# Kernel tuning notes

Measured on AMD Instinct MI355X. Metric: run time of the kernel, lower is better.

## Reference

```python
import jax, jax.numpy as jnp
import numpy as np
import math

B, S, D, H = 2, 2048, 1024, 16
HD = D // H
WINDOW_LEFT = 256   # window_size=(256,-1): only left constraint active
NEG = -1e9


def rotate_half(x):
    x1, x2 = jnp.split(x, 2, axis=-1)
    return jnp.concatenate([-x2, x1], axis=-1)


def setup_inputs() -> dict:
    key = jax.random.key(0)
    ks = jax.random.split(key, 10)
    x = jax.random.normal(ks[0], (B, S, D), dtype=jnp.float32)
    mask = jnp.ones((B, S), dtype=bool)
    cos = jax.random.uniform(ks[1], (B, S, HD), dtype=jnp.float32)
    sin = jax.random.uniform(ks[2], (B, S, HD), dtype=jnp.float32)
    sc = 1.0 / math.sqrt(D)
    Wq = jax.random.normal(ks[3], (D, D), dtype=jnp.float32) * sc
    bq = jax.random.normal(ks[4], (D,), dtype=jnp.float32) * 0.02
    Wk = jax.random.normal(ks[5], (D, D), dtype=jnp.float32) * sc
    Wv = jax.random.normal(ks[6], (D, D), dtype=jnp.float32) * sc
    bv = jax.random.normal(ks[7], (D,), dtype=jnp.float32) * 0.02
    Wo = jax.random.normal(ks[8], (D, D), dtype=jnp.float32) * sc
    bo = jax.random.normal(ks[9], (D,), dtype=jnp.float32) * 0.02
    return {"x": x, "mask": mask, "cos": cos, "sin": sin,
            "Wq": Wq, "bq": bq, "Wk": Wk, "Wv": Wv, "bv": bv,
            "Wo": Wo, "bo": bo}


def reference(x, mask, cos, sin, Wq, bq, Wk, Wv, bv, Wo, bo):
    batch, seq_len, embed_dim = x.shape
    scale = 1.0 / math.sqrt(HD)

    q = x @ Wq + bq          # [b,s,d], bias on q
    k = x @ Wk               # no bias on k
    v = x @ Wv + bv          # bias on v

    def split_heads(t):
        return jnp.swapaxes(t.reshape(batch, seq_len, H, HD), 1, 2)  # [b,h,s,hd]

    q, k, v = split_heads(q), split_heads(k), split_heads(v)

    c = cos[:, None, :, :]   # [b,1,s,hd]
    s_ = sin[:, None, :, :]
    q = q * c + rotate_half(q) * s_
    k = k * c + rotate_half(k) * s_

    scores = jnp.einsum('bhqd,bhkd->bhqk', q, k) * scale
    # padding mask over keys
    scores = jnp.where(mask[:, None, None, :], scores, NEG)
    # causal + sliding-window (left=256) masks combined
    pos = jnp.arange(seq_len)
    rel = pos[None, :] - pos[:, None]          # k - q
    keep = (rel <= 0) & (rel >= -WINDOW_LEFT)  # causal AND window-left
    scores = jnp.where(keep, scores, NEG)

    weights = jax.nn.softmax(scores, axis=-1)
    context = jnp.einsum('bhqk,bhkd->bhqd', weights, v)
    context = jnp.swapaxes(context, 1, 2).reshape(batch, seq_len, embed_dim)
    out = context @ Wo + bo
    out = out * mask[..., None]
    return out
```

## Files before the change

### kernel.cpp

```cpp
#include <hip/hip_runtime.h>
#include <cstdint>
#include <cstddef>

typedef __bf16 bf16;
typedef bf16 bf16x4 __attribute__((ext_vector_type(4)));
typedef bf16 bf16x8 __attribute__((ext_vector_type(8)));
typedef float f32x4 __attribute__((ext_vector_type(4)));

#define S_LEN 2048
#define DIM   1024
#define NHEAD 16
#define HDIM  64

__device__ __forceinline__ f32x4 mfma16(bf16x8 a, bf16x8 b, f32x4 c) {
    return __builtin_amdgcn_mfma_f32_16x16x32_bf16(a, b, c, 0, 0, 0);
}

__device__ __forceinline__ float exp2fast(float x) {
    return __builtin_amdgcn_exp2f(x);
}

__device__ __forceinline__ void gload_lds16(const bf16* g, bf16* l) {
    __builtin_amdgcn_global_load_lds(
        (const __attribute__((address_space(1))) unsigned*)g,
        (__attribute__((address_space(3))) unsigned*)l, 16, 0, 0);
}

__global__ __launch_bounds__(256) void cvt_x_kernel(const float* __restrict__ x,
                                                    bf16* __restrict__ xb) {
    int i = blockIdx.x * 256 + threadIdx.x;
    float4 v = ((const float4*)x)[i];
    bf16x4 o = { (bf16)v.x, (bf16)v.y, (bf16)v.z, (bf16)v.w };
    ((bf16x4*)xb)[i] = o;
}

__global__ __launch_bounds__(256) void wt_kernel(const float* __restrict__ Wq, const float* __restrict__ Wk,
                                                 const float* __restrict__ Wv, const float* __restrict__ Wo,
                                                 bf16* __restrict__ WqT, bf16* __restrict__ WkT,
                                                 bf16* __restrict__ WvT, bf16* __restrict__ WoT) {
    const float* W; bf16* WT;
    int z = blockIdx.z;
    if      (z == 0) { W = Wq; WT = WqT; }
    else if (z == 1) { W = Wk; WT = WkT; }
    else if (z == 2) { W = Wv; WT = WvT; }
    else             { W = Wo; WT = WoT; }
    __shared__ bf16 tile[64][72];
    int k0 = blockIdx.x * 64, n0 = blockIdx.y * 64;
    int t = threadIdx.x;
#pragma unroll
    for (int p = 0; p < 4; ++p) {
        int task = p * 256 + t;
        int ki = task >> 4, nj = (task & 15) * 4;
        float4 v = *(const float4*)(W + (size_t)(k0 + ki) * DIM + n0 + nj);
        tile[ki][nj + 0] = (bf16)v.x; tile[ki][nj + 1] = (bf16)v.y;
        tile[ki][nj + 2] = (bf16)v.z; tile[ki][nj + 3] = (bf16)v.w;
    }
    __syncthreads();
#pragma unroll
    for (int p = 0; p < 4; ++p) {
        int task = p * 256 + t;
        int ni = task >> 4, kj = (task & 15) * 4;
        bf16x4 o = { tile[kj + 0][ni], tile[kj + 1][ni], tile[kj + 2][ni], tile[kj + 3][ni] };
        *(bf16x4*)(WT + (size_t)(n0 + ni) * DIM + k0 + kj) = o;
    }
}

__device__ __forceinline__ void stage_tile(const bf16* __restrict__ A, const bf16* __restrict__ BT,
                                           int m0, int n0, int k0,
                                           bf16* sA, bf16* sB, int w, int lane) {
#pragma unroll
    for (int p = 0; p < 2; ++p) {
        int c = p * 256 + w * 64 + lane;
        const bf16* ga = A + (size_t)(m0 + (c >> 2)) * DIM + k0 + (c & 3) * 8;
        gload_lds16(ga, sA + (p * 256 + w * 64) * 8);
        const bf16* gb = BT + (size_t)(n0 + (c >> 2)) * DIM + k0 + (c & 3) * 8;
        gload_lds16(gb, sB + (p * 256 + w * 64) * 8);
    }
}

__device__ __forceinline__ void gemm_main(const bf16* __restrict__ A, const bf16* __restrict__ BT,
                                          int m0, int n0, f32x4 acc[4][4]) {
    __shared__ bf16 sA[3][128 * 32];
    __shared__ bf16 sB[3][128 * 32];
    int t = threadIdx.x;
    int lane = t & 63, w = t >> 6;
    int wr = w >> 1, wc = w & 1;
    int lc = lane & 15, lr = lane >> 4;
    const int NSTEP = DIM / 32;

    stage_tile(A, BT, m0, n0, 0,  sA[0], sB[0], w, lane);
    stage_tile(A, BT, m0, n0, 32, sA[1], sB[1], w, lane);

    int rs = 0, ss = 2;
    for (int kt = 0; kt < NSTEP; ++kt) {
        if (kt < NSTEP - 1) asm volatile("s_waitcnt vmcnt(4)" ::: "memory");
        else                asm volatile("s_waitcnt vmcnt(0)" ::: "memory");
        __builtin_amdgcn_s_barrier();
        asm volatile("" ::: "memory");
        if (kt < NSTEP - 2)
            stage_tile(A, BT, m0, n0, (kt + 2) * 32, sA[ss], sB[ss], w, lane);

        const bf16* pa = sA[rs] + (wr * 64 + lc) * 32 + lr * 8;
        const bf16* pb = sB[rs] + (wc * 64 + lc) * 32 + lr * 8;
        bf16x8 af[4], bfr[4];
#pragma unroll
        for (int m = 0; m < 4; ++m) af[m] = *(const bf16x8*)(pa + m * 16 * 32);
#pragma unroll
        for (int n = 0; n < 4; ++n) bfr[n] = *(const bf16x8*)(pb + n * 16 * 32);
#pragma unroll
        for (int m = 0; m < 4; ++m)
#pragma unroll
            for (int n = 0; n < 4; ++n)
                acc[m][n] = mfma16(af[m], bfr[n], acc[m][n]);
        rs = (rs == 2) ? 0 : rs + 1;
        ss = (ss == 2) ? 0 : ss + 1;
    }
}

__global__ __launch_bounds__(256, 3) void gemm_qkv_kernel(const bf16* __restrict__ xb,
                                                          const bf16* __restrict__ WqT, const bf16* __restrict__ WkT,
                                                          const bf16* __restrict__ WvT,
                                                          const float* __restrict__ bq, const float* __restrict__ bv,
                                                          const float* __restrict__ cosp, const float* __restrict__ sinp,
                                                          bf16* __restrict__ qT, bf16* __restrict__ kT,
                                                          bf16* __restrict__ vT) {
    int z = blockIdx.z;
    const bf16* BT = (z == 0) ? WqT : (z == 1) ? WkT : WvT;
    int m0 = blockIdx.x * 128, n0 = blockIdx.y * 128;
    f32x4 acc[4][4] = {};
    gemm_main(xb, BT, m0, n0, acc);

    int t = threadIdx.x;
    int lane = t & 63, w = t >> 6;
    int wr = w >> 1, wc = w & 1;
    int lc = lane & 15, lr = lane >> 4;
    int row0 = m0 + wr * 64 + lr * 4;
    int h = (n0 >> 6) + wc;

    if (z < 2) {
        bf16* qkT = (z == 0) ? qT : kT;
#pragma unroll
        for (int nf = 0; nf < 2; ++nf) {
            int hd1 = lc + nf * 16;
            int c1i = h * HDIM + hd1;
            float b1 = (z == 0) ? bq[c1i] : 0.0f;
            float b2 = (z == 0) ? bq[c1i + 32] : 0.0f;
#pragma unroll
            for (int mf = 0; mf < 4; ++mf) {
#pragma unroll
                for (int r = 0; r < 4; ++r) {
                    int bs = row0 + mf * 16 + r;
                    size_t cb = (size_t)bs * HDIM + hd1;
                    float c1 = cosp[cb], s1 = sinp[cb];
                    float c2 = cosp[cb + 32], s2 = sinp[cb + 32];
                    float v1 = acc[mf][nf][r] + b1;
                    float v2 = acc[mf][nf + 2][r] + b2;
                    int b = bs >> 11, s = bs & (S_LEN - 1);
                    size_t o = ((size_t)(b * NHEAD + h) * S_LEN + s) * HDIM;
                    qkT[o + hd1]      = (bf16)(v1 * c1 - v2 * s1);
                    qkT[o + hd1 + 32] = (bf16)(v2 * c2 + v1 * s2);
                }
            }
        }
    } else {
#pragma unroll
        for (int nf = 0; nf < 4; ++nf) {
            int hd = lc + nf * 16;
            float bvv = bv[h * HDIM + hd];
#pragma unroll
            for (int mf = 0; mf < 4; ++mf) {
                bf16x4 o;
#pragma unroll
                for (int r = 0; r < 4; ++r) o[r] = (bf16)(acc[mf][nf][r] + bvv);
                int bs = row0 + mf * 16;
                int b = bs >> 11, s = bs & (S_LEN - 1);
                *(bf16x4*)(vT + ((size_t)((b * NHEAD + h) * HDIM + hd)) * S_LEN + s) = o;
            }
        }
    }
}

__global__ __launch_bounds__(256, 3) void gemm_out_kernel(const bf16* __restrict__ ctx, const bf16* __restrict__ WoT,
                                                          const float* __restrict__ bo, float* __restrict__ out) {
    int m0 = blockIdx.x * 128, n0 = blockIdx.y * 128;
    f32x4 acc[4][4] = {};
    gemm_main(ctx, WoT, m0, n0, acc);
    int t = threadIdx.x;
    int lane = t & 63, w = t >> 6;
    int wr = w >> 1, wc = w & 1;
    int lc = lane & 15, lr = lane >> 4;
    int row0 = m0 + wr * 64 + lr * 4;
    int col0 = n0 + wc * 64 + lc;
#pragma unroll
    for (int nf = 0; nf < 4; ++nf) {
        int col = col0 + nf * 16;
        float bvv = bo[col];
#pragma unroll
        for (int mf = 0; mf < 4; ++mf)
#pragma unroll
            for (int r = 0; r < 4; ++r)
                out[(size_t)(row0 + mf * 16 + r) * DIM + col] = acc[mf][nf][r] + bvv;
    }
}

__global__ __launch_bounds__(64) void attn_kernel(const bf16* __restrict__ qT, const bf16* __restrict__ kT,
                                                  const bf16* __restrict__ vT, bf16* __restrict__ ctx) {
    int q0 = blockIdx.x * 32;
    int bh = blockIdx.y;
    int b = bh >> 4, h = bh & 15;
    int lane = threadIdx.x;
    int lc = lane & 15, lr = lane >> 4;
    __shared__ bf16 sP[32 * 64];
    const bf16* Qb = qT + (size_t)bh * S_LEN * HDIM;
    const bf16* Kb = kT + (size_t)bh * S_LEN * HDIM;
    const bf16* Vb = vT + (size_t)bh * HDIM * S_LEN;

    const float SCL = 0.125f * 1.44269504089f;

    bf16x8 qf[2][2];
#pragma unroll
    for (int mf = 0; mf < 2; ++mf)
#pragma unroll
        for (int kk = 0; kk < 2; ++kk)
            qf[mf][kk] = *(const bf16x8*)(Qb + (size_t)(q0 + mf * 16 + lc) * HDIM + kk * 32 + lr * 8);

    f32x4 accO[2][4] = {};
    float mrun[2] = { -30000.0f, -30000.0f };
    float lrun[2] = { 0.0f, 0.0f };

    int klo = (q0 >= 256) ? ((q0 - 256) >> 6) : 0;
    int khi = (q0 + 31) >> 6;
    for (int kt = klo; kt <= khi; ++kt) {
        int kbase = kt * 64;
        f32x4 sacc[2][4] = {};
        __builtin_amdgcn_s_setprio(1);
#pragma unroll
        for (int nf = 0; nf < 4; ++nf)
#pragma unroll
            for (int kk = 0; kk < 2; ++kk) {
                bf16x8 kf = *(const bf16x8*)(Kb + (size_t)(kbase + nf * 16 + lc) * HDIM + kk * 32 + lr * 8);
                sacc[0][nf] = mfma16(kf, qf[0][kk], sacc[0][nf]);
                sacc[1][nf] = mfma16(kf, qf[1][kk], sacc[1][nf]);
            }
        __builtin_amdgcn_s_setprio(0);
        float p[2][4][4];
#pragma unroll
        for (int mf = 0; mf < 2; ++mf) {
            int qi = q0 + mf * 16 + lc;
#pragma unroll
            for (int nf = 0; nf < 4; ++nf)
#pragma unroll
                for (int r = 0; r < 4; ++r) {
                    int ki = kbase + nf * 16 + lr * 4 + r;
                    bool keep = (ki <= qi) && (ki >= qi - 256);
                    p[mf][nf][r] = keep ? sacc[mf][nf][r] * SCL : -30000.0f;
                }
        }
#pragma unroll
        for (int mf = 0; mf < 2; ++mf) {
            float mx = p[mf][0][0];
#pragma unroll
            for (int nf = 0; nf < 4; ++nf)
#pragma unroll
                for (int r = 0; r < 4; ++r) mx = fmaxf(mx, p[mf][nf][r]);
            mx = fmaxf(mx, __shfl_xor(mx, 16));
            mx = fmaxf(mx, __shfl_xor(mx, 32));
            float mnew = fmaxf(mrun[mf], mx);
            float alpha = exp2fast(mrun[mf] - mnew);
            mrun[mf] = mnew;
            float rs = 0.0f;
#pragma unroll
            for (int nf = 0; nf < 4; ++nf)
#pragma unroll
                for (int r = 0; r < 4; ++r) {
                    float e = exp2fast(p[mf][nf][r] - mnew);
                    p[mf][nf][r] = e;
                    rs += e;
                }
            rs += __shfl_xor(rs, 16);
            rs += __shfl_xor(rs, 32);
            lrun[mf] = lrun[mf] * alpha + rs;
            float aq[4];
#pragma unroll
            for (int r = 0; r < 4; ++r) aq[r] = __shfl(alpha, lr * 4 + r);
#pragma unroll
            for (int n4 = 0; n4 < 4; ++n4)
#pragma unroll
                for (int r = 0; r < 4; ++r) accO[mf][n4][r] *= aq[r];
        }
#pragma unroll
        for (int mf = 0; mf < 2; ++mf)
#pragma unroll
            for (int nf = 0; nf < 4; ++nf) {
                bf16x4 o = { (bf16)p[mf][nf][0], (bf16)p[mf][nf][1],
                             (bf16)p[mf][nf][2], (bf16)p[mf][nf][3] };
                *(bf16x4*)(sP + (mf * 16 + lc) * 64 + nf * 16 + lr * 4) = o;
            }
        asm volatile("s_waitcnt lgkmcnt(0)" ::: "memory");
        bf16x8 pf[2][2];
#pragma unroll
        for (int mf = 0; mf < 2; ++mf)
#pragma unroll
            for (int kk = 0; kk < 2; ++kk)
                pf[mf][kk] = *(const bf16x8*)(sP + (mf * 16 + lc) * 64 + kk * 32 + lr * 8);
        __builtin_amdgcn_s_setprio(1);
#pragma unroll
        for (int n4 = 0; n4 < 4; ++n4)
#pragma unroll
            for (int kk = 0; kk < 2; ++kk) {
                bf16x8 vf = *(const bf16x8*)(Vb + (size_t)(n4 * 16 + lc) * S_LEN + kbase + kk * 32 + lr * 8);
                accO[0][n4] = mfma16(pf[0][kk], vf, accO[0][n4]);
                accO[1][n4] = mfma16(pf[1][kk], vf, accO[1][n4]);
            }
        __builtin_amdgcn_s_setprio(0);
    }
#pragma unroll
    for (int mf = 0; mf < 2; ++mf) {
        float linv = 1.0f / lrun[mf];
        float lq[4];
#pragma unroll
        for (int r = 0; r < 4; ++r) lq[r] = __shfl(linv, lr * 4 + r);
#pragma unroll
        for (int n4 = 0; n4 < 4; ++n4)
#pragma unroll
            for (int r = 0; r < 4; ++r) {
                int s = q0 + mf * 16 + lr * 4 + r;
                int d = n4 * 16 + lc;
                ctx[((size_t)(b * S_LEN + s)) * DIM + h * HDIM + d] = (bf16)(accO[mf][n4][r] * lq[r]);
            }
    }
}

extern "C" void kernel_launch(void* const* d_in, const int* in_sizes, int n_in,
                              void* d_out, int out_size, void* d_ws, size_t ws_size,
                              hipStream_t stream) {
    const float* x    = (const float*)d_in[0];
    const float* cosp = (const float*)d_in[2];
    const float* sinp = (const float*)d_in[3];
    const float* Wq   = (const float*)d_in[4];
    const float* bq   = (const float*)d_in[5];
    const float* Wk   = (const float*)d_in[6];
    const float* Wv   = (const float*)d_in[7];
    const float* bv   = (const float*)d_in[8];
    const float* Wo   = (const float*)d_in[9];
    const float* bo   = (const float*)d_in[10];
    float* out = (float*)d_out;

    char* ws = (char*)d_ws;
    const size_t MB = 1ull << 20;
    bf16* xb  = (bf16*)(ws + 0 * MB);
    bf16* WqT = (bf16*)(ws + 8 * MB);
    bf16* WkT = (bf16*)(ws + 10 * MB);
    bf16* WvT = (bf16*)(ws + 12 * MB);
    bf16* WoT = (bf16*)(ws + 14 * MB);
    bf16* qT  = (bf16*)(ws + 16 * MB);
    bf16* kT  = (bf16*)(ws + 24 * MB);
    bf16* vT  = (bf16*)(ws + 32 * MB);
    bf16* ctx = (bf16*)(ws + 40 * MB);

    cvt_x_kernel<<<4096, 256, 0, stream>>>(x, xb);
    wt_kernel<<<dim3(16, 16, 4), 256, 0, stream>>>(Wq, Wk, Wv, Wo, WqT, WkT, WvT, WoT);
    gemm_qkv_kernel<<<dim3(32, 8, 3), 256, 0, stream>>>(xb, WqT, WkT, WvT, bq, bv, cosp, sinp, qT, kT, vT);
    attn_kernel<<<dim3(64, 32), 64, 0, stream>>>(qT, kT, vT, ctx);
    gemm_out_kernel<<<dim3(32, 8), 256, 0, stream>>>(ctx, WoT, bo, out);
}
```

Measured before the change: 107.0 us.

## Prefetch next K tile and current V tile into registers; swizzle P in LDS

The attention loop now issues the V loads for the current tile and the K loads for the next tile at the top of each iteration, holding them in register arrays. This lets global-memory latency overlap with the QK MFMAs and the softmax instead of stalling right before each use. It also XOR-swizzles the byte addresses of the P staging buffer in shared memory to cut LDS bank conflicts. In exchange the kernel holds about 24 extra 128-bit values in registers, which could raise register pressure, reduce occupancy, or cause spilling.

```diff
diff --git a/kernel.cpp b/kernel.cpp
--- a/kernel.cpp
+++ b/kernel.cpp
@@ -211,11 +211,13 @@
     int lane = threadIdx.x;
     int lc = lane & 15, lr = lane >> 4;
     __shared__ bf16 sP[32 * 64];
+    char* sPb = (char*)sP;
     const bf16* Qb = qT + (size_t)bh * S_LEN * HDIM;
     const bf16* Kb = kT + (size_t)bh * S_LEN * HDIM;
     const bf16* Vb = vT + (size_t)bh * HDIM * S_LEN;
 
     const float SCL = 0.125f * 1.44269504089f;
+    const int swz = (lc & 7) << 4;
 
     bf16x8 qf[2][2];
 #pragma unroll
@@ -230,20 +232,39 @@
 
     int klo = (q0 >= 256) ? ((q0 - 256) >> 6) : 0;
     int khi = (q0 + 31) >> 6;
+
+    bf16x8 kfc[8], kfn[8], vf[8];
+#pragma unroll
+    for (int nf = 0; nf < 4; ++nf)
+#pragma unroll
+        for (int kk = 0; kk < 2; ++kk)
+            kfc[nf * 2 + kk] = *(const bf16x8*)(Kb + (size_t)(klo * 64 + nf * 16 + lc) * HDIM + kk * 32 + lr * 8);
+
     for (int kt = klo; kt <= khi; ++kt) {
         int kbase = kt * 64;
+#pragma unroll
+        for (int n4 = 0; n4 < 4; ++n4)
+#pragma unroll
+            for (int kk = 0; kk < 2; ++kk)
+                vf[n4 * 2 + kk] = *(const bf16x8*)(Vb + (size_t)(n4 * 16 + lc) * S_LEN + kbase + kk * 32 + lr * 8);
+        if (kt < khi) {
+#pragma unroll
+            for (int nf = 0; nf < 4; ++nf)
+#pragma unroll
+                for (int kk = 0; kk < 2; ++kk)
+                    kfn[nf * 2 + kk] = *(const bf16x8*)(Kb + (size_t)(kbase + 64 + nf * 16 + lc) * HDIM + kk * 32 + lr * 8);
+        }
+
         f32x4 sacc[2][4] = {};
         __builtin_amdgcn_s_setprio(1);
 #pragma unroll
         for (int nf = 0; nf < 4; ++nf)
 #pragma unroll
             for (int kk = 0; kk < 2; ++kk) {
-                bf16x8 kf = *(const bf16x8*)(Kb + (size_t)(kbase + nf * 16 + lc) * HDIM + kk * 32 + lr * 8);
-                sacc[0][nf] = mfma16(kf, qf[0][kk], sacc[0][nf]);
-                sacc[1][nf] = mfma16(kf, qf[1][kk], sacc[1][nf]);
+                sacc[0][nf] = mfma16(kfc[nf * 2 + kk], qf[0][kk], sacc[0][nf]);
+                sacc[1][nf] = mfma16(kfc[nf * 2 + kk], qf[1][kk], sacc[1][nf]);
             }
         __builtin_amdgcn_s_setprio(0);
-        float p[2][4][4];
 #pragma unroll
         for (int mf = 0; mf < 2; ++mf) {
             int qi = q0 + mf * 16 + lc;
@@ -253,33 +274,33 @@
                 for (int r = 0; r < 4; ++r) {
                     int ki = kbase + nf * 16 + lr * 4 + r;
                     bool keep = (ki <= qi) && (ki >= qi - 256);
-                    p[mf][nf][r] = keep ? sacc[mf][nf][r] * SCL : -30000.0f;
+                    sacc[mf][nf][r] = keep ? sacc[mf][nf][r] * SCL : -30000.0f;
                 }
         }
 #pragma unroll
         for (int mf = 0; mf < 2; ++mf) {
-            float mx = p[mf][0][0];
+            float mx = sacc[mf][0][0];
 #pragma unroll
             for (int nf = 0; nf < 4; ++nf)
 #pragma unroll
-                for (int r = 0; r < 4; ++r) mx = fmaxf(mx, p[mf][nf][r]);
+                for (int r = 0; r < 4; ++r) mx = fmaxf(mx, sacc[mf][nf][r]);
             mx = fmaxf(mx, __shfl_xor(mx, 16));
             mx = fmaxf(mx, __shfl_xor(mx, 32));
             float mnew = fmaxf(mrun[mf], mx);
             float alpha = exp2fast(mrun[mf] - mnew);
             mrun[mf] = mnew;
-            float rs = 0.0f;
+            float rsum = 0.0f;
 #pragma unroll
             for (int nf = 0; nf < 4; ++nf)
 #pragma unroll
                 for (int r = 0; r < 4; ++r) {
-                    float e = exp2fast(p[mf][nf][r] - mnew);
-                    p[mf][nf][r] = e;
-                    rs += e;
+                    float e = exp2fast(sacc[mf][nf][r] - mnew);
+                    sacc[mf][nf][r] = e;
+                    rsum += e;
                 }
-            rs += __shfl_xor(rs, 16);
-            rs += __shfl_xor(rs, 32);
-            lrun[mf] = lrun[mf] * alpha + rs;
+            rsum += __shfl_xor(rsum, 16);
+            rsum += __shfl_xor(rsum, 32);
+            lrun[mf] = lrun[mf] * alpha + rsum;
             float aq[4];
 #pragma unroll
             for (int r = 0; r < 4; ++r) aq[r] = __shfl(alpha, lr * 4 + r);
@@ -292,27 +313,31 @@
         for (int mf = 0; mf < 2; ++mf)
 #pragma unroll
             for (int nf = 0; nf < 4; ++nf) {
-                bf16x4 o = { (bf16)p[mf][nf][0], (bf16)p[mf][nf][1],
-                             (bf16)p[mf][nf][2], (bf16)p[mf][nf][3] };
-                *(bf16x4*)(sP + (mf * 16 + lc) * 64 + nf * 16 + lr * 4) = o;
+                bf16x4 o = { (bf16)sacc[mf][nf][0], (bf16)sacc[mf][nf][1],
+                             (bf16)sacc[mf][nf][2], (bf16)sacc[mf][nf][3] };
+                int wb = ((mf * 16 + lc) * 64 + nf * 16 + lr * 4) * 2;
+                *(bf16x4*)(sPb + (wb ^ swz)) = o;
             }
         asm volatile("s_waitcnt lgkmcnt(0)" ::: "memory");
         bf16x8 pf[2][2];
 #pragma unroll
         for (int mf = 0; mf < 2; ++mf)
 #pragma unroll
-            for (int kk = 0; kk < 2; ++kk)
-                pf[mf][kk] = *(const bf16x8*)(sP + (mf * 16 + lc) * 64 + kk * 32 + lr * 8);
+            for (int kk = 0; kk < 2; ++kk) {
+                int rb = ((mf * 16 + lc) * 64 + kk * 32 + lr * 8) * 2;
+                pf[mf][kk] = *(const bf16x8*)(sPb + (rb ^ swz));
+            }
         __builtin_amdgcn_s_setprio(1);
 #pragma unroll
         for (int n4 = 0; n4 < 4; ++n4)
 #pragma unroll
             for (int kk = 0; kk < 2; ++kk) {
-                bf16x8 vf = *(const bf16x8*)(Vb + (size_t)(n4 * 16 + lc) * S_LEN + kbase + kk * 32 + lr * 8);
-                accO[0][n4] = mfma16(pf[0][kk], vf, accO[0][n4]);
-                accO[1][n4] = mfma16(pf[1][kk], vf, accO[1][n4]);
+                accO[0][n4] = mfma16(pf[0][kk], vf[n4 * 2 + kk], accO[0][n4]);
+                accO[1][n4] = mfma16(pf[1][kk], vf[n4 * 2 + kk], accO[1][n4]);
             }
         __builtin_amdgcn_s_setprio(0);
+#pragma unroll
+        for (int i = 0; i < 8; ++i) kfc[i] = kfn[i];
     }
 #pragma unroll
     for (int mf = 0; mf < 2; ++mf) {
```

After: 104.6 us. 2.2% less time.
